# Kernel optimization log

Hardware: AMD Instinct MI355X
Metric: run time of the kernel (lower is better)

## Reference

```python
import jax, jax.numpy as jnp
import numpy as np

B, C_IN, C_OUT, N, L = 4, 128, 256, 4096, 4
D = C_OUT // 4
EPS_BN = 1e-5


def setup_inputs() -> dict:
    key = jax.random.key(0)
    ks = jax.random.split(key, 16)
    s_in = 1.0 / np.sqrt(C_IN)
    s_out = 1.0 / np.sqrt(C_OUT)
    return {
        "features": jax.random.normal(ks[0], (B, C_IN, N), dtype=jnp.float32),
        # LBR: conv1x1 -> BN -> ReLU -> conv1x1 -> BN -> ReLU
        "lbr_w1": jax.random.uniform(ks[1], (C_OUT, C_IN), jnp.float32, -s_in, s_in),
        "lbr_g1": jnp.ones((C_OUT,), jnp.float32),
        "lbr_b1": jnp.zeros((C_OUT,), jnp.float32),
        "lbr_w2": jax.random.uniform(ks[2], (C_OUT, C_OUT), jnp.float32, -s_out, s_out),
        "lbr_g2": jnp.ones((C_OUT,), jnp.float32),
        "lbr_b2": jnp.zeros((C_OUT,), jnp.float32),
        # per-layer OffsetAttention params (stacked on leading L axis)
        # q_conv and k_conv share the same weight (q_conv.weight = k_conv.weight)
        "attn_qk_w": jax.random.uniform(ks[3], (L, D, C_OUT), jnp.float32, -s_out, s_out),
        "attn_v_w": jax.random.uniform(ks[4], (L, C_OUT, C_OUT), jnp.float32, -s_out, s_out),
        "attn_v_b": jax.random.uniform(ks[5], (L, C_OUT), jnp.float32, -s_out, s_out),
        "attn_t_w": jax.random.uniform(ks[6], (L, C_OUT, C_OUT), jnp.float32, -s_out, s_out),
        "attn_t_b": jax.random.uniform(ks[7], (L, C_OUT), jnp.float32, -s_out, s_out),
        "attn_bn_g": jnp.ones((L, C_OUT), jnp.float32),
        "attn_bn_b": jnp.zeros((L, C_OUT), jnp.float32),
    }


def batchnorm1d(x, gamma, beta):
    # x: [B, C, N]; training-mode BN: batch stats over (B, N), biased variance
    mean = jnp.mean(x, axis=(0, 2), keepdims=True)
    var = jnp.mean(jnp.square(x - mean), axis=(0, 2), keepdims=True)
    xn = (x - mean) * jax.lax.rsqrt(var + EPS_BN)
    return xn * gamma[None, :, None] + beta[None, :, None]


def offset_attention(x, qk_w, v_w, v_b, t_w, t_b, bn_g, bn_b):
    # x: [B, C, N]
    K = jnp.einsum("dc,bcn->bdn", qk_w, x)            # [B, D, N]
    # Q = same conv, permuted to [B, N, D]; attention_map = Q @ K -> [B, N, N]
    attn = jnp.einsum("bdn,bdm->bnm", K, K)
    attn = jax.nn.softmax(attn, axis=-1)
    # extra L1 renorm over dim=1 (column-wise)
    attn = attn / (1e-9 + jnp.sum(attn, axis=1, keepdims=True))
    V = jnp.einsum("dc,bcn->bdn", v_w, x) + v_b[None, :, None]  # [B, C, N]
    new_feat = jnp.einsum("bcn,bnm->bcm", V, attn)    # [B, C, N]
    off = x - new_feat
    t = jnp.einsum("dc,bcn->bdn", t_w, off) + t_b[None, :, None]
    return jax.nn.relu(batchnorm1d(t, bn_g, bn_b))


def reference(features, lbr_w1, lbr_g1, lbr_b1, lbr_w2, lbr_g2, lbr_b2,
              attn_qk_w, attn_v_w, attn_v_b, attn_t_w, attn_t_b,
              attn_bn_g, attn_bn_b):
    # LBR stem
    h = jnp.einsum("dc,bcn->bdn", lbr_w1, features)
    h = jax.nn.relu(batchnorm1d(h, lbr_g1, lbr_b1))
    h = jnp.einsum("dc,bcn->bdn", lbr_w2, h)
    h = jax.nn.relu(batchnorm1d(h, lbr_g2, lbr_b2))
    # stacked offset attention; output concatenates attention outputs only
    outs = []
    cur = h
    for i in range(L):
        cur = offset_attention(cur, attn_qk_w[i], attn_v_w[i], attn_v_b[i],
                               attn_t_w[i], attn_t_b[i], attn_bn_g[i], attn_bn_b[i])
        outs.append(cur)
    return jnp.concatenate(outs, axis=1)  # [B, C_OUT*L, N]
```

## Files before the change

### kernel.cpp

```cpp
#include <hip/hip_runtime.h>
#include <hip/hip_bf16.h>
#include <math.h>

#define NPTS 4096
#define CO   256
#define CI   128
#define BB   4
#define DQ   64
#define LL   4
#define PST  136

typedef __attribute__((ext_vector_type(8))) short bf16x8;
typedef __attribute__((ext_vector_type(4))) float f32x4;

#define MFMA16(a,b,c) __builtin_amdgcn_mfma_f32_16x16x32_bf16((a),(b),(c),0,0,0)

__device__ __forceinline__ short fb(float x) {
  __hip_bfloat16 h = __float2bfloat16(x);
  return __builtin_bit_cast(short, h);
}
__device__ __forceinline__ float bf(short s) {
  unsigned u = ((unsigned)(unsigned short)s) << 16;
  return __builtin_bit_cast(float, u);
}

__global__ __launch_bounds__(256) void cvtw_k(
    const float* __restrict__ S, short* __restrict__ D, int n8)
{
  const int i = blockIdx.x * 256 + threadIdx.x;
  if (i < n8) {
    const float4 a = ((const float4*)S)[i * 2];
    const float4 b = ((const float4*)S)[i * 2 + 1];
    bf16x8 r;
    r[0] = fb(a.x); r[1] = fb(a.y); r[2] = fb(a.z); r[3] = fb(a.w);
    r[4] = fb(b.x); r[5] = fb(b.y); r[6] = fb(b.z); r[7] = fb(b.w);
    ((bf16x8*)D)[i] = r;
  }
}

__global__ __launch_bounds__(256) void tcvt_k(
    const float* __restrict__ X, long xbs, int C, short* __restrict__ XT)
{
  const int n0 = blockIdx.x * 64, c0 = blockIdx.y * 64, b = blockIdx.z;
  const int t = threadIdx.x, tl = t & 63, tg = t >> 6;
  __shared__ float xs[64][65];
#pragma unroll
  for (int r = 0; r < 16; ++r) {
    const int cc = tg * 16 + r;
    xs[cc][tl] = X[(long)b * xbs + (long)(c0 + cc) * NPTS + n0 + tl];
  }
  __syncthreads();
#pragma unroll
  for (int r = 0; r < 16; ++r) {
    const int nn = tg * 16 + r;
    XT[((long)b * NPTS + n0 + nn) * C + c0 + tl] = fb(xs[tl][nn]);
  }
}

template<int OMODE, bool BIAS>
__global__ __launch_bounds__(256) void conv_a(
    const short* __restrict__ XT, int C,
    const short* __restrict__ Wb, const float* __restrict__ bias,
    void* __restrict__ Yv, long ybs)
{
  const int n0 = blockIdx.x * 128, d0 = blockIdx.y * 64, b = blockIdx.z;
  const int tid = threadIdx.x, w = tid >> 6, l = tid & 63, lg = l >> 4, lr = l & 15;
  const short* xb = XT + (long)b * NPTS * C;
  f32x4 acc[8];
#pragma unroll
  for (int i = 0; i < 8; ++i) acc[i] = (f32x4){0.f, 0.f, 0.f, 0.f};
  const int dr = d0 + w * 16 + lr;
  for (int kc = 0; kc < C; kc += 32) {
    const bf16x8 af = *(const bf16x8*)&Wb[(long)dr * C + kc + lg * 8];
#pragma unroll
    for (int ni = 0; ni < 8; ++ni) {
      const bf16x8 bx = *(const bf16x8*)&xb[(long)(n0 + ni * 16 + lr) * C + kc + lg * 8];
      acc[ni] = MFMA16(af, bx, acc[ni]);
    }
  }
  float bv[4] = {0.f, 0.f, 0.f, 0.f};
  if (BIAS) {
    const float4 b4 = *(const float4*)&bias[d0 + w * 16 + lg * 4];
    bv[0] = b4.x; bv[1] = b4.y; bv[2] = b4.z; bv[3] = b4.w;
  }
  const int db = d0 + w * 16 + lg * 4;
#pragma unroll
  for (int ni = 0; ni < 8; ++ni) {
    const int n = n0 + ni * 16 + lr;
#pragma unroll
    for (int j = 0; j < 4; ++j) {
      const float o = acc[ni][j] + bv[j];
      if constexpr (OMODE == 0) {
        ((float*)Yv)[(long)b * ybs + (long)(db + j) * NPTS + n] = o;
      } else {
        ((short*)Yv)[(long)b * ybs + ((long)(n0 >> 7) * CO + db + j) * 128 + (n & 127)] = fb(o);
      }
    }
  }
}

__global__ __launch_bounds__(256) void conv_b(
    const short* __restrict__ XT, const short* __restrict__ Wb,
    short* __restrict__ KTo)
{
  const int n0 = blockIdx.x * 64, b = blockIdx.y;
  const int tid = threadIdx.x, w = tid >> 6, l = tid & 63, lg = l >> 4, lr = l & 15;
  const short* xb = XT + (long)b * NPTS * CO;
  f32x4 acc[4];
#pragma unroll
  for (int i = 0; i < 4; ++i) acc[i] = (f32x4){0.f, 0.f, 0.f, 0.f};
  const long nr = n0 + w * 16 + lr;
  for (int kc = 0; kc < CO; kc += 32) {
    const bf16x8 af = *(const bf16x8*)&xb[nr * CO + kc + lg * 8];
#pragma unroll
    for (int di = 0; di < 4; ++di) {
      const bf16x8 wf = *(const bf16x8*)&Wb[(long)(di * 16 + lr) * CO + kc + lg * 8];
      acc[di] = MFMA16(af, wf, acc[di]);
    }
  }
  short* Ko = KTo + (long)b * NPTS * DQ;
  const int nb = n0 + w * 16 + lg * 4;
#pragma unroll
  for (int j = 0; j < 4; ++j) {
#pragma unroll
    for (int di = 0; di < 4; ++di)
      Ko[(long)(nb + j) * DQ + di * 16 + lr] = fb(acc[di][j]);
  }
}

__global__ __launch_bounds__(256) void bnstats_k(
    const float* __restrict__ X, long xbs,
    float* __restrict__ mean, float* __restrict__ rstd)
{
  const int c = blockIdx.x, t = threadIdx.x;
  float s = 0.f, s2 = 0.f;
  for (int b = 0; b < BB; ++b) {
    const float4* p = (const float4*)(X + (long)b * xbs + (long)c * NPTS);
    for (int n = t; n < NPTS / 4; n += 256) {
      const float4 v = p[n];
      s  += v.x + v.y + v.z + v.w;
      s2 += v.x * v.x + v.y * v.y + v.z * v.z + v.w * v.w;
    }
  }
#pragma unroll
  for (int o = 32; o > 0; o >>= 1) { s += __shfl_down(s, o); s2 += __shfl_down(s2, o); }
  __shared__ float a1[4], a2[4];
  if ((t & 63) == 0) { a1[t >> 6] = s; a2[t >> 6] = s2; }
  __syncthreads();
  if (t == 0) {
    const float S  = a1[0] + a1[1] + a1[2] + a1[3];
    const float S2 = a2[0] + a2[1] + a2[2] + a2[3];
    const float m  = S / (float)(BB * NPTS);
    const float v  = S2 / (float)(BB * NPTS) - m * m;
    mean[c] = m;
    rstd[c] = rsqrtf(v + 1e-5f);
  }
}

template<bool WF32, bool WBF>
__global__ __launch_bounds__(256) void bnrelu_t(
    const float* __restrict__ X, long xbs,
    const float* __restrict__ mean, const float* __restrict__ rstd,
    const float* __restrict__ g, const float* __restrict__ be,
    float* __restrict__ Yf, long ybs, short* __restrict__ XT)
{
  const int n0 = blockIdx.x * 64, c0 = blockIdx.y * 64, b = blockIdx.z;
  const int t = threadIdx.x, tl = t & 63, tg = t >> 6;
  __shared__ float xs[64][65];
#pragma unroll
  for (int r = 0; r < 16; ++r) {
    const int cc = tg * 16 + r, c = c0 + cc;
    float v = X[(long)b * xbs + (long)c * NPTS + n0 + tl];
    v = fmaxf((v - mean[c]) * rstd[c] * g[c] + be[c], 0.f);
    if (WF32) Yf[(long)b * ybs + (long)c * NPTS + n0 + tl] = v;
    xs[cc][tl] = v;
  }
  __syncthreads();
  if (WBF) {
#pragma unroll
    for (int r = 0; r < 16; ++r) {
      const int nn = tg * 16 + r;
      XT[((long)b * NPTS + n0 + nn) * CO + c0 + tl] = fb(xs[tl][nn]);
    }
  }
}

#define ONL(MX, SM, SV) { const float m2_ = fmaxf(MX, SV); \
  SM = SM * __expf(MX - m2_) + __expf(SV - m2_); MX = m2_; }
#define MRG(MX, SM, OFF) { const float om_ = __shfl_xor(MX, OFF); \
  const float os_ = __shfl_xor(SM, OFF); \
  const float m2_ = fmaxf(MX, om_); \
  SM = SM * __expf(MX - m2_) + os_ * __expf(om_ - m2_); MX = m2_; }

__global__ __launch_bounds__(256) void rowstats_mfma(
    const short* __restrict__ KT, float* __restrict__ pmax, float* __restrict__ psum)
{
  const int bid = blockIdx.x;
  const int b = (bid >> 1) & 3;
  const int idx = (bid >> 3) * 2 + (bid & 1);
  const int n0 = (idx & 63) * 64;
  const int chunk = idx >> 6;
  const int tid = threadIdx.x, w = tid >> 6, l = tid & 63, lg = l >> 4, lr = l & 15;
  const short* Kb = KT + (long)b * NPTS * DQ;
  const int nr = n0 + w * 16 + lr;
  const bf16x8 a0 = *(const bf16x8*)&Kb[(long)nr * DQ + lg * 8];
  const bf16x8 a1 = *(const bf16x8*)&Kb[(long)nr * DQ + 32 + lg * 8];

  float mx0 = -INFINITY, mx1 = -INFINITY, mx2 = -INFINITY, mx3 = -INFINITY;
  float sm0 = 0.f, sm1 = 0.f, sm2 = 0.f, sm3 = 0.f;

  const int mc = chunk * (NPTS / 4);
  for (int m0 = mc; m0 < mc + NPTS / 4; m0 += 16) {
    const bf16x8 b0 = *(const bf16x8*)&Kb[(long)(m0 + lr) * DQ + lg * 8];
    const bf16x8 b1 = *(const bf16x8*)&Kb[(long)(m0 + lr) * DQ + 32 + lg * 8];
    f32x4 s = {0.f, 0.f, 0.f, 0.f};
    s = MFMA16(a0, b0, s);
    s = MFMA16(a1, b1, s);
    ONL(mx0, sm0, s[0]); ONL(mx1, sm1, s[1]);
    ONL(mx2, sm2, s[2]); ONL(mx3, sm3, s[3]);
  }
#pragma unroll
  for (int off = 1; off < 16; off <<= 1) {
    MRG(mx0, sm0, off); MRG(mx1, sm1, off);
    MRG(mx2, sm2, off); MRG(mx3, sm3, off);
  }
  if (lr == 0) {
    const long base = ((long)chunk * BB + b) * NPTS + n0 + w * 16 + lg * 4;
    pmax[base + 0] = mx0; pmax[base + 1] = mx1; pmax[base + 2] = mx2; pmax[base + 3] = mx3;
    psum[base + 0] = sm0; psum[base + 1] = sm1; psum[base + 2] = sm2; psum[base + 3] = sm3;
  }
}

__global__ __launch_bounds__(256) void combine_k(
    const float* __restrict__ pmax, const float* __restrict__ psum,
    float* __restrict__ rmax, float* __restrict__ rinv)
{
  const long i = (long)blockIdx.x * 256 + threadIdx.x;
  const long st = (long)BB * NPTS;
  float m = pmax[i];
  m = fmaxf(m, pmax[st + i]); m = fmaxf(m, pmax[2 * st + i]); m = fmaxf(m, pmax[3 * st + i]);
  const float s = psum[i] * __expf(pmax[i] - m)
                + psum[st + i] * __expf(pmax[st + i] - m)
                + psum[2 * st + i] * __expf(pmax[2 * st + i] - m)
                + psum[3 * st + i] * __expf(pmax[3 * st + i] - m);
  rmax[i] = m;
  rinv[i] = 1.f / s;
}

__global__ __launch_bounds__(512) void pass2_mfma(
    const short* __restrict__ KT, const short* __restrict__ Vblk,
    const float* __restrict__ rmax, const float* __restrict__ rinv,
    short* __restrict__ XO)
{
  const int bid = blockIdx.x;
  const int b  = (bid >> 1) & 3;
  const int m0 = ((bid >> 3) * 2 + (bid & 1)) * 64;
  const int tid = threadIdx.x;
  const int w = tid >> 6, l = tid & 63, lg = l >> 4, lr = l & 15;

  const short* Kb = KT + (long)b * NPTS * DQ;
  const short* Vb = Vblk + (long)b * CO * NPTS;
  const float* rmb = rmax + (long)b * NPTS;
  const float* rib = rinv + (long)b * NPTS;

  __shared__ short Ps[2][64][PST];
  __shared__ float cspart[8][64];
  __shared__ float csum[64];

  bf16x8 bK[4][2];
#pragma unroll
  for (int ms = 0; ms < 4; ++ms) {
    bK[ms][0] = *(const bf16x8*)&Kb[(long)(m0 + ms * 16 + lr) * DQ + lg * 8];
    bK[ms][1] = *(const bf16x8*)&Kb[(long)(m0 + ms * 16 + lr) * DQ + 32 + lg * 8];
  }

  f32x4 acc[4][2];
#pragma unroll
  for (int i = 0; i < 4; ++i) {
    acc[i][0] = (f32x4){0.f, 0.f, 0.f, 0.f};
    acc[i][1] = (f32x4){0.f, 0.f, 0.f, 0.f};
  }
  float cs[4] = {0.f, 0.f, 0.f, 0.f};
  const int c0 = w * 32;
  const int nb = w * 16;

  bf16x8 a0 = *(const bf16x8*)&Kb[(long)(nb + lr) * DQ + lg * 8];
  bf16x8 a1 = *(const bf16x8*)&Kb[(long)(nb + lr) * DQ + 32 + lg * 8];
  float4 rm4 = *(const float4*)&rmb[nb + lg * 4];
  float4 ri4 = *(const float4*)&rib[nb + lg * 4];

  int buf = 0;
  for (int n0 = 0; n0 < NPTS; n0 += 128) {
    const short* vt = Vb + (long)(n0 >> 7) * CO * 128;
    bf16x8 vf[4][2];
#pragma unroll
    for (int kc = 0; kc < 4; ++kc) {
      vf[kc][0] = *(const bf16x8*)&vt[(long)(c0 + lr) * 128 + kc * 32 + lg * 8];
      vf[kc][1] = *(const bf16x8*)&vt[(long)(c0 + 16 + lr) * 128 + kc * 32 + lg * 8];
    }
    f32x4 s[4];
#pragma unroll
    for (int ms = 0; ms < 4; ++ms) {
      s[ms] = (f32x4){0.f, 0.f, 0.f, 0.f};
      s[ms] = MFMA16(a0, bK[ms][0], s[ms]);
      s[ms] = MFMA16(a1, bK[ms][1], s[ms]);
    }
#pragma unroll
    for (int ms = 0; ms < 4; ++ms) {
      const float p0 = __expf(s[ms][0] - rm4.x) * ri4.x;
      const float p1 = __expf(s[ms][1] - rm4.y) * ri4.y;
      const float p2 = __expf(s[ms][2] - rm4.z) * ri4.z;
      const float p3 = __expf(s[ms][3] - rm4.w) * ri4.w;
      cs[ms] += p0 + p1 + p2 + p3;
      const unsigned u0 = ((unsigned)(unsigned short)fb(p1) << 16) | (unsigned short)fb(p0);
      const unsigned u1 = ((unsigned)(unsigned short)fb(p3) << 16) | (unsigned short)fb(p2);
      *(uint2*)&Ps[buf][ms * 16 + lr][nb + lg * 4] = make_uint2(u0, u1);
    }
    asm volatile("s_waitcnt lgkmcnt(0)" ::: "memory");
    __builtin_amdgcn_s_barrier();
    if (n0 + 128 < NPTS) {
      a0 = *(const bf16x8*)&Kb[(long)(n0 + 128 + nb + lr) * DQ + lg * 8];
      a1 = *(const bf16x8*)&Kb[(long)(n0 + 128 + nb + lr) * DQ + 32 + lg * 8];
      rm4 = *(const float4*)&rmb[n0 + 128 + nb + lg * 4];
      ri4 = *(const float4*)&rib[n0 + 128 + nb + lg * 4];
    }
#pragma unroll
    for (int kc = 0; kc < 4; ++kc) {
      bf16x8 pa[4];
#pragma unroll
      for (int ms = 0; ms < 4; ++ms)
        pa[ms] = *(const bf16x8*)&Ps[buf][ms * 16 + lr][kc * 32 + lg * 8];
#pragma unroll
      for (int ms = 0; ms < 4; ++ms) {
        acc[ms][0] = MFMA16(pa[ms], vf[kc][0], acc[ms][0]);
        acc[ms][1] = MFMA16(pa[ms], vf[kc][1], acc[ms][1]);
      }
    }
    buf ^= 1;
  }

  __syncthreads();
#pragma unroll
  for (int ms = 0; ms < 4; ++ms) {
    float csv = cs[ms];
    csv += __shfl_xor(csv, 16); csv += __shfl_xor(csv, 32);
    if (lg == 0) cspart[w][ms * 16 + lr] = csv;
  }
  __syncthreads();
  if (tid < 64) {
    float s = 0.f;
#pragma unroll
    for (int ww = 0; ww < 8; ++ww) s += cspart[ww][tid];
    csum[tid] = s;
  }
  __syncthreads();

  short* XOb = XO + (long)b * NPTS * CO;
#pragma unroll
  for (int ms = 0; ms < 4; ++ms) {
#pragma unroll
    for (int j = 0; j < 4; ++j) {
      const int m = m0 + ms * 16 + lg * 4 + j;
      const float inv = 1.f / (1e-9f + csum[ms * 16 + lg * 4 + j]);
      const long i0 = (long)m * CO + c0 + lr;
      const long i1 = (long)m * CO + c0 + 16 + lr;
      XOb[i0] = fb(bf(XOb[i0]) - acc[ms][0][j] * inv);
      XOb[i1] = fb(bf(XOb[i1]) - acc[ms][1][j] * inv);
    }
  }
}

extern "C" void kernel_launch(void* const* d_in, const int* in_sizes, int n_in,
                              void* d_out, int out_size, void* d_ws, size_t ws_size,
                              hipStream_t stream)
{
  const float* feat = (const float*)d_in[0];
  const float* w1   = (const float*)d_in[1];
  const float* g1   = (const float*)d_in[2];
  const float* b1   = (const float*)d_in[3];
  const float* w2   = (const float*)d_in[4];
  const float* g2   = (const float*)d_in[5];
  const float* b2   = (const float*)d_in[6];
  const float* qkw  = (const float*)d_in[7];
  const float* vw   = (const float*)d_in[8];
  const float* vb   = (const float*)d_in[9];
  const float* tw   = (const float*)d_in[10];
  const float* tb   = (const float*)d_in[11];
  const float* bng  = (const float*)d_in[12];
  const float* bnb  = (const float*)d_in[13];

  float* out = (float*)d_out;

  short* xt    = (short*)d_ws;
  short* KTb   = xt + (long)BB * NPTS * CO;
  short* Vblk  = KTb + (long)BB * NPTS * DQ;
  short* wb1   = Vblk + (long)BB * CO * NPTS;
  short* wb2   = wb1 + (long)CO * CI;
  short* wqk   = wb2 + (long)CO * CO;
  short* wv    = wqk + (long)LL * DQ * CO;
  short* wt    = wv + (long)LL * CO * CO;
  float* pmaxb = (float*)(wt + (long)LL * CO * CO);
  float* psumb = pmaxb + (long)4 * BB * NPTS;
  float* rmaxb = psumb + (long)4 * BB * NPTS;
  float* rinvb = rmaxb + (long)BB * NPTS;
  float* meanb = rinvb + (long)BB * NPTS;
  float* rstdb = meanb + CO;

  const long OBS = (long)LL * CO * NPTS;
  float* h1 = out + (long)2 * CO * NPTS;
  float* x0 = out + (long)1 * CO * NPTS;

  const dim3 blk(256);

  cvtw_k<<<dim3((CO * CI / 8 + 255) / 256), blk, 0, stream>>>(w1, wb1, CO * CI / 8);
  cvtw_k<<<dim3((CO * CO / 8 + 255) / 256), blk, 0, stream>>>(w2, wb2, CO * CO / 8);
  cvtw_k<<<dim3((LL * DQ * CO / 8 + 255) / 256), blk, 0, stream>>>(qkw, wqk, LL * DQ * CO / 8);
  cvtw_k<<<dim3((LL * CO * CO / 8 + 255) / 256), blk, 0, stream>>>(vw, wv, LL * CO * CO / 8);
  cvtw_k<<<dim3((LL * CO * CO / 8 + 255) / 256), blk, 0, stream>>>(tw, wt, LL * CO * CO / 8);

  tcvt_k<<<dim3(64, 2, BB), blk, 0, stream>>>(feat, (long)CI * NPTS, CI, xt);
  conv_a<0, false><<<dim3(32, 4, BB), blk, 0, stream>>>(xt, CI, wb1, nullptr, h1, OBS);
  bnstats_k<<<dim3(CO), blk, 0, stream>>>(h1, OBS, meanb, rstdb);
  bnrelu_t<false, true><<<dim3(64, 4, BB), blk, 0, stream>>>(
      h1, OBS, meanb, rstdb, g1, b1, nullptr, 0, xt);
  conv_a<0, false><<<dim3(32, 4, BB), blk, 0, stream>>>(xt, CO, wb2, nullptr, x0, OBS);
  bnstats_k<<<dim3(CO), blk, 0, stream>>>(x0, OBS, meanb, rstdb);
  bnrelu_t<false, true><<<dim3(64, 4, BB), blk, 0, stream>>>(
      x0, OBS, meanb, rstdb, g2, b2, nullptr, 0, xt);

  for (int lyr = 0; lyr < LL; ++lyr) {
    float* nft = out + (long)lyr * CO * NPTS;
    conv_b<<<dim3(64, BB), blk, 0, stream>>>(xt, wqk + (long)lyr * DQ * CO, KTb);
    conv_a<1, true><<<dim3(32, 4, BB), blk, 0, stream>>>(
        xt, CO, wv + (long)lyr * CO * CO, vb + (long)lyr * CO, Vblk, (long)CO * NPTS);
    rowstats_mfma<<<dim3(1024), blk, 0, stream>>>(KTb, pmaxb, psumb);
    combine_k<<<dim3(BB * NPTS / 256), blk, 0, stream>>>(pmaxb, psumb, rmaxb, rinvb);
    pass2_mfma<<<dim3(256), dim3(512), 0, stream>>>(KTb, Vblk, rmaxb, rinvb, xt);
    conv_a<0, true><<<dim3(32, 4, BB), blk, 0, stream>>>(
        xt, CO, wt + (long)lyr * CO * CO, tb + (long)lyr * CO, nft, OBS);
    bnstats_k<<<dim3(CO), blk, 0, stream>>>(nft, OBS, meanb, rstdb);
    if (lyr < LL - 1) {
      bnrelu_t<true, true><<<dim3(64, 4, BB), blk, 0, stream>>>(
          nft, OBS, meanb, rstdb, bng + (long)lyr * CO, bnb + (long)lyr * CO, nft, OBS, xt);
    } else {
      bnrelu_t<true, false><<<dim3(64, 4, BB), blk, 0, stream>>>(
          nft, OBS, meanb, rstdb, bng + (long)lyr * CO, bnb + (long)lyr * CO, nft, OBS, nullptr);
    }
  }
}
```

Baseline: 911.2 us.

## Software-pipeline P computation in pass2 and split online softmax accumulators in rowstats

In pass2, the score/exp block for the next tile is now computed and written to the alternate LDS buffer while the current tile's P fragments are being consumed by the PV MFMAs. This overlaps exp work with matrix work and needs one barrier per iteration. In rowstats, each thread now keeps four independent online max/sum accumulators and processes 64 columns per iteration. The update is branchless and uses a single exp instead of two, which shortens the serial dependency chain. The cost is higher register pressure in both kernels, since all P fragments are preloaded into registers.

After: 949.3 us. 4.2% more time.

```diff
diff --git a/kernel.cpp b/kernel.cpp
--- a/kernel.cpp
+++ b/kernel.cpp
@@ -184,13 +184,6 @@
     }
   }
 }
-
-#define ONL(MX, SM, SV) { const float m2_ = fmaxf(MX, SV); \
-  SM = SM * __expf(MX - m2_) + __expf(SV - m2_); MX = m2_; }
-#define MRG(MX, SM, OFF) { const float om_ = __shfl_xor(MX, OFF); \
-  const float os_ = __shfl_xor(SM, OFF); \
-  const float m2_ = fmaxf(MX, om_); \
-  SM = SM * __expf(MX - m2_) + os_ * __expf(om_ - m2_); MX = m2_; }
 
 __global__ __launch_bounds__(256) void rowstats_mfma(
     const short* __restrict__ KT, float* __restrict__ pmax, float* __restrict__ psum)
@@ -206,19 +199,46 @@
   const bf16x8 a0 = *(const bf16x8*)&Kb[(long)nr * DQ + lg * 8];
   const bf16x8 a1 = *(const bf16x8*)&Kb[(long)nr * DQ + 32 + lg * 8];
 
-  float mx0 = -INFINITY, mx1 = -INFINITY, mx2 = -INFINITY, mx3 = -INFINITY;
-  float sm0 = 0.f, sm1 = 0.f, sm2 = 0.f, sm3 = 0.f;
+  float mx[4][4], sm[4][4];
+#pragma unroll
+  for (int p = 0; p < 4; ++p)
+#pragma unroll
+    for (int j = 0; j < 4; ++j) { mx[p][j] = -INFINITY; sm[p][j] = 0.f; }
 
   const int mc = chunk * (NPTS / 4);
-  for (int m0 = mc; m0 < mc + NPTS / 4; m0 += 16) {
-    const bf16x8 b0 = *(const bf16x8*)&Kb[(long)(m0 + lr) * DQ + lg * 8];
-    const bf16x8 b1 = *(const bf16x8*)&Kb[(long)(m0 + lr) * DQ + 32 + lg * 8];
-    f32x4 s = {0.f, 0.f, 0.f, 0.f};
-    s = MFMA16(a0, b0, s);
-    s = MFMA16(a1, b1, s);
-    ONL(mx0, sm0, s[0]); ONL(mx1, sm1, s[1]);
-    ONL(mx2, sm2, s[2]); ONL(mx3, sm3, s[3]);
-  }
+  for (int m0 = mc; m0 < mc + NPTS / 4; m0 += 64) {
+#pragma unroll
+    for (int p = 0; p < 4; ++p) {
+      const bf16x8 b0 = *(const bf16x8*)&Kb[(long)(m0 + p * 16 + lr) * DQ + lg * 8];
+      const bf16x8 b1 = *(const bf16x8*)&Kb[(long)(m0 + p * 16 + lr) * DQ + 32 + lg * 8];
+      f32x4 s = {0.f, 0.f, 0.f, 0.f};
+      s = MFMA16(a0, b0, s);
+      s = MFMA16(a1, b1, s);
+#pragma unroll
+      for (int j = 0; j < 4; ++j) {
+        const float d = s[j] - mx[p][j];
+        const float e = __expf(-fabsf(d));
+        const bool gt = d > 0.f;
+        sm[p][j] = gt ? fmaf(sm[p][j], e, 1.f) : (sm[p][j] + e);
+        mx[p][j] = gt ? s[j] : mx[p][j];
+      }
+    }
+  }
+#pragma unroll
+  for (int p = 1; p < 4; ++p)
+#pragma unroll
+    for (int j = 0; j < 4; ++j) {
+      const float m2 = fmaxf(mx[0][j], mx[p][j]);
+      sm[0][j] = sm[0][j] * __expf(mx[0][j] - m2) + sm[p][j] * __expf(mx[p][j] - m2);
+      mx[0][j] = m2;
+    }
+
+  float mx0 = mx[0][0], mx1 = mx[0][1], mx2 = mx[0][2], mx3 = mx[0][3];
+  float sm0 = sm[0][0], sm1 = sm[0][1], sm2 = sm[0][2], sm3 = sm[0][3];
+#define MRG(MX, SM, OFF) { const float om_ = __shfl_xor(MX, OFF); \
+  const float os_ = __shfl_xor(SM, OFF); \
+  const float m2_ = fmaxf(MX, om_); \
+  SM = SM * __expf(MX - m2_) + os_ * __expf(om_ - m2_); MX = m2_; }
 #pragma unroll
   for (int off = 1; off < 16; off <<= 1) {
     MRG(mx0, sm0, off); MRG(mx1, sm1, off);
@@ -257,6 +277,7 @@
   const int m0 = ((bid >> 3) * 2 + (bid & 1)) * 64;
   const int tid = threadIdx.x;
   const int w = tid >> 6, l = tid & 63, lg = l >> 4, lr = l & 15;
+  const int NT = NPTS / 128;
 
   const short* Kb = KT + (long)b * NPTS * DQ;
   const short* Vb = Vblk + (long)b * CO * NPTS;
@@ -284,20 +305,10 @@
   const int c0 = w * 32;
   const int nb = w * 16;
 
-  bf16x8 a0 = *(const bf16x8*)&Kb[(long)(nb + lr) * DQ + lg * 8];
-  bf16x8 a1 = *(const bf16x8*)&Kb[(long)(nb + lr) * DQ + 32 + lg * 8];
-  float4 rm4 = *(const float4*)&rmb[nb + lg * 4];
-  float4 ri4 = *(const float4*)&rib[nb + lg * 4];
-
-  int buf = 0;
-  for (int n0 = 0; n0 < NPTS; n0 += 128) {
-    const short* vt = Vb + (long)(n0 >> 7) * CO * 128;
-    bf16x8 vf[4][2];
-#pragma unroll
-    for (int kc = 0; kc < 4; ++kc) {
-      vf[kc][0] = *(const bf16x8*)&vt[(long)(c0 + lr) * 128 + kc * 32 + lg * 8];
-      vf[kc][1] = *(const bf16x8*)&vt[(long)(c0 + 16 + lr) * 128 + kc * 32 + lg * 8];
-    }
+  bf16x8 a0, a1;
+  float4 rm4, ri4;
+
+  auto sblk = [&](int dbuf) {
     f32x4 s[4];
 #pragma unroll
     for (int ms = 0; ms < 4; ++ms) {
@@ -314,29 +325,56 @@
       cs[ms] += p0 + p1 + p2 + p3;
       const unsigned u0 = ((unsigned)(unsigned short)fb(p1) << 16) | (unsigned short)fb(p0);
       const unsigned u1 = ((unsigned)(unsigned short)fb(p3) << 16) | (unsigned short)fb(p2);
-      *(uint2*)&Ps[buf][ms * 16 + lr][nb + lg * 4] = make_uint2(u0, u1);
-    }
+      *(uint2*)&Ps[dbuf][ms * 16 + lr][nb + lg * 4] = make_uint2(u0, u1);
+    }
+  };
+
+  a0  = *(const bf16x8*)&Kb[(long)(nb + lr) * DQ + lg * 8];
+  a1  = *(const bf16x8*)&Kb[(long)(nb + lr) * DQ + 32 + lg * 8];
+  rm4 = *(const float4*)&rmb[nb + lg * 4];
+  ri4 = *(const float4*)&rib[nb + lg * 4];
+  sblk(0);
+  a0  = *(const bf16x8*)&Kb[(long)(128 + nb + lr) * DQ + lg * 8];
+  a1  = *(const bf16x8*)&Kb[(long)(128 + nb + lr) * DQ + 32 + lg * 8];
+  rm4 = *(const float4*)&rmb[128 + nb + lg * 4];
+  ri4 = *(const float4*)&rib[128 + nb + lg * 4];
+
+  for (int i = 0; i < NT; ++i) {
+    const int n0 = i * 128;
     asm volatile("s_waitcnt lgkmcnt(0)" ::: "memory");
     __builtin_amdgcn_s_barrier();
-    if (n0 + 128 < NPTS) {
-      a0 = *(const bf16x8*)&Kb[(long)(n0 + 128 + nb + lr) * DQ + lg * 8];
-      a1 = *(const bf16x8*)&Kb[(long)(n0 + 128 + nb + lr) * DQ + 32 + lg * 8];
-      rm4 = *(const float4*)&rmb[n0 + 128 + nb + lg * 4];
-      ri4 = *(const float4*)&rib[n0 + 128 + nb + lg * 4];
-    }
+
+    const short* vt = Vb + (long)(n0 >> 7) * CO * 128;
+    bf16x8 vf[4][2];
 #pragma unroll
     for (int kc = 0; kc < 4; ++kc) {
-      bf16x8 pa[4];
+      vf[kc][0] = *(const bf16x8*)&vt[(long)(c0 + lr) * 128 + kc * 32 + lg * 8];
+      vf[kc][1] = *(const bf16x8*)&vt[(long)(c0 + 16 + lr) * 128 + kc * 32 + lg * 8];
+    }
+    bf16x8 pa[4][4];
+#pragma unroll
+    for (int kc = 0; kc < 4; ++kc)
 #pragma unroll
       for (int ms = 0; ms < 4; ++ms)
-        pa[ms] = *(const bf16x8*)&Ps[buf][ms * 16 + lr][kc * 32 + lg * 8];
+        pa[ms][kc] = *(const bf16x8*)&Ps[i & 1][ms * 16 + lr][kc * 32 + lg * 8];
+
+    if (i + 1 < NT) {
+      sblk((i + 1) & 1);
+      if (i + 2 < NT) {
+        a0  = *(const bf16x8*)&Kb[(long)((i + 2) * 128 + nb + lr) * DQ + lg * 8];
+        a1  = *(const bf16x8*)&Kb[(long)((i + 2) * 128 + nb + lr) * DQ + 32 + lg * 8];
+        rm4 = *(const float4*)&rmb[(i + 2) * 128 + nb + lg * 4];
+        ri4 = *(const float4*)&rib[(i + 2) * 128 + nb + lg * 4];
+      }
+    }
+
+#pragma unroll
+    for (int kc = 0; kc < 4; ++kc)
 #pragma unroll
       for (int ms = 0; ms < 4; ++ms) {
-        acc[ms][0] = MFMA16(pa[ms], vf[kc][0], acc[ms][0]);
-        acc[ms][1] = MFMA16(pa[ms], vf[kc][1], acc[ms][1]);
+        acc[ms][0] = MFMA16(pa[ms][kc], vf[kc][0], acc[ms][0]);
+        acc[ms][1] = MFMA16(pa[ms][kc], vf[kc][1], acc[ms][1]);
       }
-    }
-    buf ^= 1;
   }
 
   __syncthreads();
```
